# Performance work log

Measured on AMD Instinct MI355X. Metric: run time of the kernel, lower is better.

Reference implementation:

```python
import jax, jax.numpy as jnp
import numpy as np
from jax import lax

N_QUBITS = 8
DIM = 256  # 2**8 amplitudes
NUM_BLOCKS = 16
DEPTH = 1
ALPHA = 0.5
BATCH = 512

# Z-sign tables: qubit 0 is the most-significant bit of the flattened state index
_bits = (np.arange(DIM)[:, None] >> (N_QUBITS - 1 - np.arange(N_QUBITS))) & 1  # (256, 8)
_SIGNS = jnp.asarray(1.0 - 2.0 * _bits, dtype=jnp.float32)  # (256, 8)
_pairs = [(i, j) for i in range(N_QUBITS) for j in range(i + 1, N_QUBITS)]
_PAIR_SIGNS = jnp.stack([_SIGNS[:, i] * _SIGNS[:, j] for (i, j) in _pairs], axis=1)  # (256, 28)


def _apply_ry(state, c, s, q):
    # state: (N, 256) real (RY and CNOT keep the state real); gate on qubit q
    dl, dr = 2 ** q, 2 ** (N_QUBITS - 1 - q)
    st = state.reshape(-1, dl, 2, dr)
    s0, s1 = st[:, :, 0, :], st[:, :, 1, :]
    c_, s_ = c[:, None, None], s[:, None, None]
    n0 = c_ * s0 - s_ * s1
    n1 = s_ * s0 + c_ * s1
    return jnp.stack([n0, n1], axis=2).reshape(-1, DIM)


def _apply_cnot_chain(state, i):
    # CNOT control=i, target=i+1 (adjacent qubits)
    dl, dr = 2 ** i, 2 ** (N_QUBITS - 2 - i)
    st = state.reshape(-1, dl, 2, 2, dr)
    c0 = st[:, :, 0]                  # control=0: unchanged
    c1 = st[:, :, 1][:, :, ::-1]      # control=1: flip target bit
    return jnp.stack([c0, c1], axis=2).reshape(-1, DIM)


def _quantum_map(theta):
    # theta: (N, 8) -> (N, 36) [Z_i expectations (8) then Z_i Z_j for i<j (28)]
    half = 0.5 * theta
    c, s = jnp.cos(half), jnp.sin(half)
    state = jnp.zeros((theta.shape[0], DIM), dtype=theta.dtype).at[:, 0].set(1.0)
    for q in range(N_QUBITS):
        state = _apply_ry(state, c[:, q], s[:, q], q)
    for _ in range(DEPTH):
        for i in range(N_QUBITS - 1):
            state = _apply_cnot_chain(state, i)
    p = state * state  # probabilities (state is real)
    single = p @ _SIGNS          # (N, 8)
    two_body = p @ _PAIR_SIGNS   # (N, 28)
    return jnp.concatenate([single, two_body], axis=1)


def _bn(x, g, b, m, v):
    # inference-mode BatchNorm2d, eps=1e-5
    inv = g / jnp.sqrt(v + 1e-5)
    return x * inv[None, :, None, None] + (b - m * inv)[None, :, None, None]


def _conv(x, w, b):
    y = lax.conv_general_dilated(x, w, (1, 1), 'SAME',
                                 dimension_numbers=('NCHW', 'OIHW', 'NCHW'))
    return y + b[None, :, None, None]


def _maxpool2(x):
    return lax.reduce_window(x, -jnp.inf, lax.max, (1, 1, 2, 2), (1, 1, 2, 2), 'VALID')


def setup_inputs() -> dict:
    key = jax.random.key(0)
    ks = jax.random.split(key, 8)
    f32 = jnp.float32
    return {
        'x': jax.random.normal(ks[0], (BATCH, 3, 64, 64), dtype=f32),
        'conv1_w': jax.random.normal(ks[1], (16, 3, 3, 3), dtype=f32) * 0.1,
        'conv1_b': jnp.zeros((16,), f32),
        'bn1_g': jnp.ones((16,), f32), 'bn1_b': jnp.zeros((16,), f32),
        'bn1_m': jnp.zeros((16,), f32), 'bn1_v': jnp.ones((16,), f32),
        'conv2_w': jax.random.normal(ks[2], (32, 16, 3, 3), dtype=f32) * 0.08,
        'conv2_b': jnp.zeros((32,), f32),
        'bn2_g': jnp.ones((32,), f32), 'bn2_b': jnp.zeros((32,), f32),
        'bn2_m': jnp.zeros((32,), f32), 'bn2_v': jnp.ones((32,), f32),
        'conv3_w': jax.random.normal(ks[3], (64, 32, 3, 3), dtype=f32) * 0.06,
        'conv3_b': jnp.zeros((64,), f32),
        'bn3_g': jnp.ones((64,), f32), 'bn3_b': jnp.zeros((64,), f32),
        'bn3_m': jnp.zeros((64,), f32), 'bn3_v': jnp.ones((64,), f32),
        'proj_w': jax.random.normal(ks[4], (NUM_BLOCKS, 256, N_QUBITS), dtype=f32) * 0.06,
        'proj_b': jnp.zeros((NUM_BLOCKS, N_QUBITS), f32),
        'cls_w': jax.random.normal(ks[5], (10, NUM_BLOCKS * 36), dtype=f32) * 0.04,
        'cls_b': jnp.zeros((10,), f32),
    }


def reference(x, conv1_w, conv1_b, bn1_g, bn1_b, bn1_m, bn1_v,
              conv2_w, conv2_b, bn2_g, bn2_b, bn2_m, bn2_v,
              conv3_w, conv3_b, bn3_g, bn3_b, bn3_m, bn3_v,
              proj_w, proj_b, cls_w, cls_b):
    h = _maxpool2(jax.nn.relu(_bn(_conv(x, conv1_w, conv1_b), bn1_g, bn1_b, bn1_m, bn1_v)))
    h = _maxpool2(jax.nn.relu(_bn(_conv(h, conv2_w, conv2_b), bn2_g, bn2_b, bn2_m, bn2_v)))
    h = _maxpool2(jax.nn.relu(_bn(_conv(h, conv3_w, conv3_b), bn3_g, bn3_b, bn3_m, bn3_v)))
    B = h.shape[0]
    feats = h.reshape(B, NUM_BLOCKS, 256)  # 16 chunks of 256
    z = jnp.einsum('bkc,kcd->bkd', feats, proj_w) + proj_b[None]  # (B, 16, 8)
    theta = ALPHA * jnp.tanh(z)
    q_out = _quantum_map(theta.reshape(B * NUM_BLOCKS, N_QUBITS))  # (B*16, 36)
    combined = q_out.reshape(B, NUM_BLOCKS * 36)
    return combined @ cls_w.T + cls_b
```

## Files before the change

### kernel.cpp

```cpp
#include <hip/hip_runtime.h>
#include <hip/hip_bf16.h>
#include <math.h>

typedef __attribute__((ext_vector_type(8))) short short8;
typedef __attribute__((ext_vector_type(4))) float f32x4;

__device__ __forceinline__ unsigned short f2bf(float f) {
    union { float f; unsigned u; } x; x.f = f;
    unsigned r = x.u + 0x7FFF + ((x.u >> 16) & 1);
    return (unsigned short)(r >> 16);
}

__device__ __forceinline__ short8 mk8(uint2 a, uint2 b) {
    union { uint2 u[2]; short8 s; } x;
    x.u[0] = a; x.u[1] = b;
    return x.s;
}

__global__ void k_prep(const float* __restrict__ w2, const float* __restrict__ w3,
    const float* g2, const float* be2, const float* m2, const float* v2, const float* cb2,
    const float* g3, const float* be3, const float* m3, const float* v3, const float* cb3,
    const float* __restrict__ w1,
    const float* g1, const float* be1, const float* m1, const float* v1, const float* cb1,
    const float* __restrict__ pjw,
    unsigned short* __restrict__ wp2, unsigned short* __restrict__ wp3,
    unsigned short* __restrict__ wp1,
    float* __restrict__ cst2, float* __restrict__ cst3, float* __restrict__ cst1,
    float* __restrict__ pjwt)
{
    int tid = blockIdx.x * 256 + threadIdx.x;
    if (tid < 5120) {
        int j = tid & 7, lane = (tid >> 3) & 63, o = (tid >> 9) & 1, s = tid >> 10;
        int kl = ((lane >> 4) << 3) + j;
        int tp = s * 2 + (kl >> 4);
        int ic = kl & 15;
        int oc = o * 16 + (lane & 15);
        float val = (tp < 9) ? w2[(oc * 16 + ic) * 9 + tp] : 0.f;
        wp2[tid] = f2bf(val);
    } else if (tid < 23552) {
        int idx = tid - 5120;
        int j = idx & 7, lane = (idx >> 3) & 63, o = (idx >> 9) & 3, tap = idx >> 11;
        int ic = ((lane >> 4) << 3) + j;
        int oc = o * 16 + (lane & 15);
        wp3[idx] = f2bf(w3[(oc * 32 + ic) * 9 + tap]);
    } else if (tid < 23648) {
        int c = tid - 23552;
        if (c < 32) {
            float inv = g2[c] * rsqrtf(v2[c] + 1e-5f);
            cst2[c] = inv;
            cst2[32 + c] = (cb2[c] - m2[c]) * inv + be2[c];
        } else {
            int c3 = c - 32;
            float inv = g3[c3] * rsqrtf(v3[c3] + 1e-5f);
            cst3[c3] = inv;
            cst3[64 + c3] = (cb3[c3] - m3[c3]) * inv + be3[c3];
        }
    } else if (tid < 24672) {
        int idx = tid - 23648;
        int j = idx & 7, lane = (idx >> 3) & 63, s = (idx >> 9) & 1;
        int k = ((lane >> 4) << 3) + j;
        int oc = lane & 15;
        float val = 0.f;
        if (s == 0) {
            int tap = k >> 2, ic = k & 3;
            if (ic < 3) val = w1[(oc * 3 + ic) * 9 + tap];
        } else {
            if (k < 3) val = w1[(oc * 3 + k) * 9 + 8];
        }
        wp1[idx] = f2bf(val);
    } else if (tid < 24688) {
        int c = tid - 24672;
        float inv = g1[c] * rsqrtf(v1[c] + 1e-5f);
        cst1[c] = inv;
        cst1[16 + c] = (cb1[c] - m1[c]) * inv + be1[c];
    } else if (tid < 57456) {
        int idx = tid - 24688;
        int k = idx >> 11, d = (idx >> 8) & 7, c = idx & 255;
        pjwt[idx] = pjw[k * 2048 + c * 8 + d];
    }
}

__global__ __launch_bounds__(512, 4) void k_fused(
    const float* __restrict__ x,
    const unsigned short* __restrict__ wp1, const float* __restrict__ cst1,
    const unsigned short* __restrict__ wp2, const float* __restrict__ cst2,
    const unsigned short* __restrict__ wp3, const float* __restrict__ cst3,
    const float* __restrict__ pjwt, const float* __restrict__ pjb,
    const float* __restrict__ cw, const float* __restrict__ cbias,
    float* __restrict__ out)
{
    __shared__ __align__(16) unsigned char smem[57728];
    unsigned short* xs   = (unsigned short*)smem;
    unsigned short* h2tA = (unsigned short*)smem;
    unsigned short* h2tB = (unsigned short*)(smem + 10368);
    unsigned short* h1A  = (unsigned short*)(smem + 20736);
    unsigned short* h1B  = (unsigned short*)(smem + 39232);
    float* feats = (float*)(smem + 20736);
    float* czs   = (float*)(smem + 20736 + 17408);
    float* partl = czs + 128;

    int b = blockIdx.x, t = threadIdx.x;
    int lane = t & 63, w = t >> 6, q = lane >> 4, xl = lane & 15;
    const float* img = x + (size_t)b * 12288;

    if (t < 264) {
        int arr = t & 1, idx = t >> 1;
        int y, xx;
        if (idx < 34)       { y = 0;        xx = idx; }
        else if (idx < 68)  { y = 33;       xx = idx - 34; }
        else if (idx < 100) { y = idx - 67; xx = 0; }
        else                { y = idx - 99; xx = 33; }
        uint4 z = {0u, 0u, 0u, 0u};
        *(uint4*)((arr ? h1B : h1A) + (y * 34 + xx) * 8) = z;
    }

    short8 A10 = *(const short8*)(wp1 + (lane << 3));
    short8 A11 = *(const short8*)(wp1 + ((64 + lane) << 3));
    int t0 = 2 * q, t1 = 2 * q + 1;
    int dy0 = t0 / 3 - 1, dx0 = t0 % 3 - 1;
    int dy1 = t1 / 3 - 1, dx1 = t1 % 3 - 1;
    float inv1[4], bs1[4];
    #pragma unroll
    for (int reg = 0; reg < 4; ++reg) {
        inv1[reg] = cst1[q * 4 + reg];
        bs1[reg]  = cst1[16 + q * 4 + reg];
    }
    unsigned* h1w = (unsigned*)(q < 2 ? h1A : h1B);
    #pragma unroll 1
    for (int h = 0; h < 2; ++h) {
        if (h) __syncthreads();
        int y0 = h * 32 - 1;
        #pragma unroll 1
        for (int i = 0; i < 5; ++i) {
            int idx = t + i * 512;
            if (idx < 2244) {
                int y = idx / 66, xx = idx - y * 66;
                int gy = y0 + y, gx = xx - 1;
                float v0 = 0.f, v1 = 0.f, v2 = 0.f;
                if ((unsigned)gy < 64u && (unsigned)gx < 64u) {
                    const float* pb = img + gy * 64 + gx;
                    v0 = pb[0]; v1 = pb[4096]; v2 = pb[8192];
                }
                uint2 pk;
                pk.x = (unsigned)f2bf(v0) | ((unsigned)f2bf(v1) << 16);
                pk.y = (unsigned)f2bf(v2);
                ((uint2*)xs)[idx] = pk;
            }
        }
        __syncthreads();
        #pragma unroll 1
        for (int xT = 0; xT < 4; ++xT) {
            int xb = xT * 16 + xl + 1;
            float pv[4], vo[4];
            #pragma unroll
            for (int r = 0; r < 4; ++r) {
                int ly = w * 4 + r + 1;
                const uint2* base = (const uint2*)xs;
                uint2 ua = base[(ly + dy0) * 66 + xb + dx0];
                uint2 ub = base[(ly + dy1) * 66 + xb + dx1];
                uint2 uc = base[(ly + 1) * 66 + xb + 1];
                f32x4 acc = (f32x4){0.f, 0.f, 0.f, 0.f};
                acc = __builtin_amdgcn_mfma_f32_16x16x32_bf16(A10, mk8(ua, ub), acc, 0, 0, 0);
                acc = __builtin_amdgcn_mfma_f32_16x16x32_bf16(A11, mk8(uc, uc), acc, 0, 0, 0);
                #pragma unroll
                for (int reg = 0; reg < 4; ++reg) {
                    float val = fmaxf(acc[reg] * inv1[reg] + bs1[reg], 0.f);
                    if (r & 1) {
                        float vm = fmaxf(val, pv[reg]);
                        vo[reg] = fmaxf(vm, __shfl_xor(vm, 1, 64));
                    } else {
                        pv[reg] = val;
                    }
                }
                if ((r & 1) && !(lane & 1)) {
                    int py = h * 16 + w * 2 + (r >> 1);
                    int px = xT * 8 + (xl >> 1);
                    int pos = (py + 1) * 34 + (px + 1);
                    unsigned u0 = (unsigned)f2bf(vo[0]) | ((unsigned)f2bf(vo[1]) << 16);
                    unsigned u1 = (unsigned)f2bf(vo[2]) | ((unsigned)f2bf(vo[3]) << 16);
                    unsigned* hp = h1w + pos * 4 + (q & 1) * 2;
                    hp[0] = u0; hp[1] = u1;
                }
            }
        }
    }
    __syncthreads();

    if (t < 264) {
        int idx = t >> 1, half = t & 1;
        int y, xx;
        if (idx < 18)      { y = 0;        xx = idx; }
        else if (idx < 36) { y = 17;       xx = idx - 18; }
        else if (idx < 52) { y = idx - 35; xx = 0; }
        else if (idx < 68) { y = idx - 51; xx = 17; }
        else { y = -1; xx = 0; }
        if (y >= 0) {
            uint4 z = {0u, 0u, 0u, 0u};
            int pos = y * 18 + xx;
            *(uint4*)((half ? h2tB : h2tA) + pos * 16) = z;
            *(uint4*)((half ? h2tB : h2tA) + pos * 16 + 8) = z;
        }
    }
    short8 A2[5][2];
    #pragma unroll
    for (int s = 0; s < 5; ++s)
        #pragma unroll
        for (int o = 0; o < 2; ++o)
            A2[s][o] = *(const short8*)(wp2 + (((s * 2 + o) * 64 + lane) << 3));
    int dyA[5], dxA[5];
    #pragma unroll
    for (int s = 0; s < 5; ++s) {
        int tp = s * 2 + (q >> 1); if (tp > 8) tp = 8;
        int d3 = tp / 3;
        dyA[s] = d3 - 1; dxA[s] = tp - d3 * 3 - 1;
    }
    {
        const unsigned short* h1r = (q & 1) ? h1B : h1A;
        f32x4 acc[4][2][2];
        #pragma unroll
        for (int r = 0; r < 4; ++r)
            #pragma unroll
            for (int xT = 0; xT < 2; ++xT)
                #pragma unroll
                for (int o = 0; o < 2; ++o)
                    acc[r][xT][o] = (f32x4){0.f, 0.f, 0.f, 0.f};
        #pragma unroll
        for (int r = 0; r < 4; ++r) {
            int ry = w * 4 + r;
            #pragma unroll
            for (int xT = 0; xT < 2; ++xT) {
                int gxb = xT * 16 + xl;
                #pragma unroll
                for (int s = 0; s < 5; ++s) {
                    int pos = (ry + dyA[s] + 1) * 34 + (gxb + dxA[s] + 1);
                    short8 B = *(const short8*)(h1r + pos * 8);
                    acc[r][xT][0] = __builtin_amdgcn_mfma_f32_16x16x32_bf16(A2[s][0], B, acc[r][xT][0], 0, 0, 0);
                    acc[r][xT][1] = __builtin_amdgcn_mfma_f32_16x16x32_bf16(A2[s][1], B, acc[r][xT][1], 0, 0, 0);
                }
            }
        }
        #pragma unroll
        for (int oT = 0; oT < 2; ++oT)
            #pragma unroll
            for (int rp = 0; rp < 2; ++rp)
                #pragma unroll
                for (int xT = 0; xT < 2; ++xT) {
                    float vo[4];
                    #pragma unroll
                    for (int reg = 0; reg < 4; ++reg) {
                        int oc = oT * 16 + q * 4 + reg;
                        float inv = cst2[oc], bs = cst2[32 + oc];
                        float v0 = fmaxf(acc[rp * 2][xT][oT][reg] * inv + bs, 0.f);
                        float v1 = fmaxf(acc[rp * 2 + 1][xT][oT][reg] * inv + bs, 0.f);
                        float vm = fmaxf(v0, v1);
                        vo[reg] = fmaxf(vm, __shfl_xor(vm, 1, 64));
                    }
                    if (!(lane & 1)) {
                        int py = w * 2 + rp;
                        int px = xT * 8 + (xl >> 1);
                        int pos = (py + 1) * 18 + (px + 1);
                        unsigned u0 = (unsigned)f2bf(vo[0]) | ((unsigned)f2bf(vo[1]) << 16);
                        unsigned u1 = (unsigned)f2bf(vo[2]) | ((unsigned)f2bf(vo[3]) << 16);
                        unsigned* hp = (unsigned*)(oT ? h2tB : h2tA) + pos * 8 + q * 2;
                        hp[0] = u0; hp[1] = u1;
                    }
                }
    }
    __syncthreads();

    {
        int op = w & 1, rg = w >> 1;
        const unsigned short* h2r = (q < 2) ? h2tA : h2tB;
        short8 A3[9][2];
        #pragma unroll
        for (int tap = 0; tap < 9; ++tap)
            #pragma unroll
            for (int tt = 0; tt < 2; ++tt)
                A3[tap][tt] = *(const short8*)(wp3 + (((tap * 4 + op * 2 + tt) * 64 + lane) << 3));
        f32x4 acc[4][2];
        #pragma unroll
        for (int r = 0; r < 4; ++r) {
            acc[r][0] = (f32x4){0.f, 0.f, 0.f, 0.f};
            acc[r][1] = (f32x4){0.f, 0.f, 0.f, 0.f};
        }
        #pragma unroll
        for (int r = 0; r < 4; ++r) {
            int ry = rg * 4 + r + 1;
            #pragma unroll
            for (int tap = 0; tap < 9; ++tap) {
                int pos = (ry + tap / 3 - 1) * 18 + xl + (tap % 3);
                short8 B = *(const short8*)(h2r + pos * 16 + (q & 1) * 8);
                acc[r][0] = __builtin_amdgcn_mfma_f32_16x16x32_bf16(A3[tap][0], B, acc[r][0], 0, 0, 0);
                acc[r][1] = __builtin_amdgcn_mfma_f32_16x16x32_bf16(A3[tap][1], B, acc[r][1], 0, 0, 0);
            }
        }
        #pragma unroll
        for (int tt = 0; tt < 2; ++tt)
            #pragma unroll
            for (int reg = 0; reg < 4; ++reg) {
                int oc = (op * 2 + tt) * 16 + q * 4 + reg;
                float inv = cst3[oc], bs = cst3[64 + oc];
                #pragma unroll
                for (int rp = 0; rp < 2; ++rp) {
                    float v0 = fmaxf(acc[rp * 2][tt][reg] * inv + bs, 0.f);
                    float v1 = fmaxf(acc[rp * 2 + 1][tt][reg] * inv + bs, 0.f);
                    float vm = fmaxf(v0, v1);
                    float vv = fmaxf(vm, __shfl_xor(vm, 1, 64));
                    if (!(lane & 1))
                        feats[oc * 68 + (rg * 2 + rp) * 8 + (xl >> 1)] = vv;
                }
            }
    }
    __syncthreads();

    if (t < 128) {
        int k = t >> 3, d = t & 7;
        const float4* wrow = (const float4*)(pjwt + (k * 8 + d) * 256);
        float zacc = 0.f;
        #pragma unroll 4
        for (int i = 0; i < 64; ++i) {
            int c4 = (i + k) & 63;
            float4 wv = wrow[c4];
            const float* fp = &feats[(k * 4 + (c4 >> 4)) * 68 + 4 * (c4 & 15)];
            float4 fv = *(const float4*)fp;
            zacc = fmaf(wv.x, fv.x, zacc);
            zacc = fmaf(wv.y, fv.y, zacc);
            zacc = fmaf(wv.z, fv.z, zacc);
            zacc = fmaf(wv.w, fv.w, zacc);
        }
        float z = zacc + pjb[k * 8 + d];
        czs[k * 8 + d] = cosf(0.5f * tanhf(z));
    }
    __syncthreads();
    if (t < 160) {
        int k = t / 10, c = t - (t / 10) * 10;
        float cz[8];
        #pragma unroll
        for (int i = 0; i < 8; ++i) cz[i] = czs[k * 8 + i];
        const float* cwp = cw + c * 576 + k * 36;
        float s = 0.f;
        float pp = 1.f;
        #pragma unroll
        for (int i = 0; i < 8; ++i) { pp *= cz[i]; s = fmaf(pp, cwp[i], s); }
        int cnt = 8;
        #pragma unroll
        for (int i = 0; i < 8; ++i) {
            float p2 = 1.f;
            #pragma unroll
            for (int j = i + 1; j < 8; ++j) { p2 *= cz[j]; s = fmaf(p2, cwp[cnt++], s); }
        }
        partl[k * 10 + c] = s;
    }
    __syncthreads();
    if (t < 10) {
        float s = cbias[t];
        #pragma unroll
        for (int k = 0; k < 16; ++k) s += partl[k * 10 + t];
        out[b * 10 + t] = s;
    }
}

extern "C" void kernel_launch(void* const* d_in, const int* in_sizes, int n_in,
                              void* d_out, int out_size, void* d_ws, size_t ws_size,
                              hipStream_t stream) {
    const float* x     = (const float*)d_in[0];
    const float* c1w   = (const float*)d_in[1];
    const float* c1b   = (const float*)d_in[2];
    const float* b1g   = (const float*)d_in[3];
    const float* b1b   = (const float*)d_in[4];
    const float* b1m   = (const float*)d_in[5];
    const float* b1v   = (const float*)d_in[6];
    const float* c2w   = (const float*)d_in[7];
    const float* c2b   = (const float*)d_in[8];
    const float* b2g   = (const float*)d_in[9];
    const float* b2b   = (const float*)d_in[10];
    const float* b2m   = (const float*)d_in[11];
    const float* b2v   = (const float*)d_in[12];
    const float* c3w   = (const float*)d_in[13];
    const float* c3b   = (const float*)d_in[14];
    const float* b3g   = (const float*)d_in[15];
    const float* b3b   = (const float*)d_in[16];
    const float* b3m   = (const float*)d_in[17];
    const float* b3v   = (const float*)d_in[18];
    const float* pjw   = (const float*)d_in[19];
    const float* pjb   = (const float*)d_in[20];
    const float* cw    = (const float*)d_in[21];
    const float* cbias = (const float*)d_in[22];
    float* outp = (float*)d_out;

    unsigned char* prep = (unsigned char*)d_ws;
    unsigned short* wp2 = (unsigned short*)prep;
    unsigned short* wp3 = (unsigned short*)(prep + 16384);
    unsigned short* wp1 = (unsigned short*)(prep + 16384 + 36864);
    float* cst2 = (float*)(prep + 16384 + 36864 + 2048);
    float* cst3 = cst2 + 64;
    float* cst1 = cst3 + 128;
    float* pjwt = (float*)(prep + 16384 + 36864 + 2048 + 1024);

    k_prep<<<225, 256, 0, stream>>>(c2w, c3w, b2g, b2b, b2m, b2v, c2b,
                                    b3g, b3b, b3m, b3v, c3b,
                                    c1w, b1g, b1b, b1m, b1v, c1b, pjw,
                                    wp2, wp3, wp1, cst2, cst3, cst1, pjwt);
    k_fused<<<512, 512, 0, stream>>>(x, wp1, cst1, wp2, cst2, wp3, cst3,
                                     pjwt, pjb, cw, cbias, outp);
}
```

Before: 138.8 us.

## Switch conv2/conv3 to 32x32x16 MFMA with channel-split layouts and transposed feats

Rewrites the conv2 and conv3 stages to use 32x32x16 bf16 MFMA tiles instead of 16x16x32. The intermediate h2 is now stored as four 8-channel planes, feats is transposed to position-major, and the projection weights are permuted to match. Weights are loaded from global per tap rather than held in registers, and the conv1 loop is unrolled by two. The aim is fewer MFMA issues and less padding waste (conv2 no longer pads 9 taps to 10), in exchange for more global weight loads and different LDS access patterns.

```diff
diff --git a/kernel.cpp b/kernel.cpp
--- a/kernel.cpp
+++ b/kernel.cpp
@@ -4,6 +4,7 @@
 
 typedef __attribute__((ext_vector_type(8))) short short8;
 typedef __attribute__((ext_vector_type(4))) float f32x4;
+typedef __attribute__((ext_vector_type(16))) float f32x16;
 
 __device__ __forceinline__ unsigned short f2bf(float f) {
     union { float f; unsigned u; } x; x.f = f;
@@ -29,22 +30,20 @@
     float* __restrict__ pjwt)
 {
     int tid = blockIdx.x * 256 + threadIdx.x;
-    if (tid < 5120) {
-        int j = tid & 7, lane = (tid >> 3) & 63, o = (tid >> 9) & 1, s = tid >> 10;
-        int kl = ((lane >> 4) << 3) + j;
-        int tp = s * 2 + (kl >> 4);
-        int ic = kl & 15;
-        int oc = o * 16 + (lane & 15);
-        float val = (tp < 9) ? w2[(oc * 16 + ic) * 9 + tp] : 0.f;
-        wp2[tid] = f2bf(val);
-    } else if (tid < 23552) {
-        int idx = tid - 5120;
-        int j = idx & 7, lane = (idx >> 3) & 63, o = (idx >> 9) & 3, tap = idx >> 11;
-        int ic = ((lane >> 4) << 3) + j;
-        int oc = o * 16 + (lane & 15);
+    if (tid < 4608) {
+        int j = tid & 7, lane = (tid >> 3) & 63, tap = tid >> 9;
+        int oc = lane & 31;
+        int ic = ((lane >> 5) << 3) + j;
+        wp2[tid] = f2bf(w2[(oc * 16 + ic) * 9 + tap]);
+    } else if (tid < 23040) {
+        int idx = tid - 4608;
+        int j = idx & 7, lane = (idx >> 3) & 63;
+        int ot = (idx >> 9) & 1, h = (idx >> 10) & 1, tap = idx >> 11;
+        int oc = ot * 32 + (lane & 31);
+        int ic = h * 16 + ((lane >> 5) << 3) + j;
         wp3[idx] = f2bf(w3[(oc * 32 + ic) * 9 + tap]);
-    } else if (tid < 23648) {
-        int c = tid - 23552;
+    } else if (tid < 23136) {
+        int c = tid - 23040;
         if (c < 32) {
             float inv = g2[c] * rsqrtf(v2[c] + 1e-5f);
             cst2[c] = inv;
@@ -55,8 +54,8 @@
             cst3[c3] = inv;
             cst3[64 + c3] = (cb3[c3] - m3[c3]) * inv + be3[c3];
         }
-    } else if (tid < 24672) {
-        int idx = tid - 23648;
+    } else if (tid < 24160) {
+        int idx = tid - 23136;
         int j = idx & 7, lane = (idx >> 3) & 63, s = (idx >> 9) & 1;
         int k = ((lane >> 4) << 3) + j;
         int oc = lane & 15;
@@ -68,15 +67,15 @@
             if (k < 3) val = w1[(oc * 3 + k) * 9 + 8];
         }
         wp1[idx] = f2bf(val);
-    } else if (tid < 24688) {
-        int c = tid - 24672;
+    } else if (tid < 24176) {
+        int c = tid - 24160;
         float inv = g1[c] * rsqrtf(v1[c] + 1e-5f);
         cst1[c] = inv;
         cst1[16 + c] = (cb1[c] - m1[c]) * inv + be1[c];
-    } else if (tid < 57456) {
-        int idx = tid - 24688;
-        int k = idx >> 11, d = (idx >> 8) & 7, c = idx & 255;
-        pjwt[idx] = pjw[k * 2048 + c * 8 + d];
+    } else if (tid < 56944) {
+        int idx = tid - 24176;
+        int o = idx & 3, pos = (idx >> 2) & 63, d = (idx >> 8) & 7, k = idx >> 11;
+        pjwt[idx] = pjw[k * 2048 + (o * 64 + pos) * 8 + d];
     }
 }
 
@@ -89,15 +88,14 @@
     const float* __restrict__ cw, const float* __restrict__ cbias,
     float* __restrict__ out)
 {
-    __shared__ __align__(16) unsigned char smem[57728];
-    unsigned short* xs   = (unsigned short*)smem;
-    unsigned short* h2tA = (unsigned short*)smem;
-    unsigned short* h2tB = (unsigned short*)(smem + 10368);
-    unsigned short* h1A  = (unsigned short*)(smem + 20736);
-    unsigned short* h1B  = (unsigned short*)(smem + 39232);
-    float* feats = (float*)(smem + 20736);
-    float* czs   = (float*)(smem + 20736 + 17408);
+    __shared__ __align__(16) unsigned char smem[58880];
+    unsigned short* xs  = (unsigned short*)smem;
+    unsigned short* h2t = (unsigned short*)smem;
+    float* czs   = (float*)(smem + 20736);
     float* partl = czs + 128;
+    unsigned short* h1A = (unsigned short*)(smem + 21888);
+    unsigned short* h1B = (unsigned short*)(smem + 40384);
+    float* feats = (float*)(smem + 21888);
 
     int b = blockIdx.x, t = threadIdx.x;
     int lane = t & 63, w = t >> 6, q = lane >> 4, xl = lane & 15;
@@ -148,7 +146,7 @@
             }
         }
         __syncthreads();
-        #pragma unroll 1
+        #pragma unroll 2
         for (int xT = 0; xT < 4; ++xT) {
             int xb = xT * 16 + xl + 1;
             float pv[4], vo[4];
@@ -186,128 +184,103 @@
     }
     __syncthreads();
 
-    if (t < 264) {
-        int idx = t >> 1, half = t & 1;
+    if (t < 272) {
+        int arr = t & 3, idx = t >> 2;
         int y, xx;
         if (idx < 18)      { y = 0;        xx = idx; }
         else if (idx < 36) { y = 17;       xx = idx - 18; }
         else if (idx < 52) { y = idx - 35; xx = 0; }
-        else if (idx < 68) { y = idx - 51; xx = 17; }
-        else { y = -1; xx = 0; }
-        if (y >= 0) {
-            uint4 z = {0u, 0u, 0u, 0u};
-            int pos = y * 18 + xx;
-            *(uint4*)((half ? h2tB : h2tA) + pos * 16) = z;
-            *(uint4*)((half ? h2tB : h2tA) + pos * 16 + 8) = z;
-        }
-    }
-    short8 A2[5][2];
-    #pragma unroll
-    for (int s = 0; s < 5; ++s)
-        #pragma unroll
-        for (int o = 0; o < 2; ++o)
-            A2[s][o] = *(const short8*)(wp2 + (((s * 2 + o) * 64 + lane) << 3));
-    int dyA[5], dxA[5];
-    #pragma unroll
-    for (int s = 0; s < 5; ++s) {
-        int tp = s * 2 + (q >> 1); if (tp > 8) tp = 8;
-        int d3 = tp / 3;
-        dyA[s] = d3 - 1; dxA[s] = tp - d3 * 3 - 1;
-    }
+        else               { y = idx - 51; xx = 17; }
+        uint4 z = {0u, 0u, 0u, 0u};
+        *(uint4*)(h2t + arr * 2592 + (y * 18 + xx) * 8) = z;
+    }
+
     {
-        const unsigned short* h1r = (q & 1) ? h1B : h1A;
-        f32x4 acc[4][2][2];
-        #pragma unroll
-        for (int r = 0; r < 4; ++r)
-            #pragma unroll
-            for (int xT = 0; xT < 2; ++xT)
+        int n = lane & 31, kh = lane >> 5;
+        const unsigned short* h1r = kh ? h1B : h1A;
+        f32x16 acc2[4];
+        #pragma unroll
+        for (int r = 0; r < 4; ++r) acc2[r] = (f32x16)(0.f);
+        #pragma unroll
+        for (int tap = 0; tap < 9; ++tap) {
+            short8 A = *(const short8*)(wp2 + ((tap * 64 + lane) << 3));
+            int dy = tap / 3 - 1, dx = tap % 3 - 1;
+            int pbase = (w * 4 + dy + 1) * 34 + (n + dx + 1);
+            #pragma unroll
+            for (int r = 0; r < 4; ++r) {
+                short8 B = *(const short8*)(h1r + (pbase + r * 34) * 8);
+                acc2[r] = __builtin_amdgcn_mfma_f32_32x32x16_bf16(A, B, acc2[r], 0, 0, 0);
+            }
+        }
+        #pragma unroll
+        for (int g = 0; g < 4; ++g) {
+            int oc0 = g * 8 + kh * 4;
+            float4 inv = *(const float4*)&cst2[oc0];
+            float4 bsv = *(const float4*)&cst2[32 + oc0];
+            #pragma unroll
+            for (int rg = 0; rg < 2; ++rg) {
+                float vo[4];
                 #pragma unroll
-                for (int o = 0; o < 2; ++o)
-                    acc[r][xT][o] = (f32x4){0.f, 0.f, 0.f, 0.f};
-        #pragma unroll
-        for (int r = 0; r < 4; ++r) {
-            int ry = w * 4 + r;
-            #pragma unroll
-            for (int xT = 0; xT < 2; ++xT) {
-                int gxb = xT * 16 + xl;
+                for (int j = 0; j < 4; ++j) {
+                    int reg = g * 4 + j;
+                    float iv = ((const float*)&inv)[j], bv = ((const float*)&bsv)[j];
+                    float v0 = fmaxf(acc2[rg * 2][reg] * iv + bv, 0.f);
+                    float v1 = fmaxf(acc2[rg * 2 + 1][reg] * iv + bv, 0.f);
+                    float vm = fmaxf(v0, v1);
+                    vo[j] = fmaxf(vm, __shfl_xor(vm, 1, 64));
+                }
+                if (!(n & 1)) {
+                    int py = w * 2 + rg, px = n >> 1;
+                    int pos = (py + 1) * 18 + (px + 1);
+                    unsigned u0 = (unsigned)f2bf(vo[0]) | ((unsigned)f2bf(vo[1]) << 16);
+                    unsigned u1 = (unsigned)f2bf(vo[2]) | ((unsigned)f2bf(vo[3]) << 16);
+                    unsigned* hp = (unsigned*)(h2t + g * 2592 + pos * 8 + kh * 4);
+                    hp[0] = u0; hp[1] = u1;
+                }
+            }
+        }
+    }
+    __syncthreads();
+
+    {
+        int n = lane & 31, kh = lane >> 5;
+        int yr = n >> 4, px_ = n & 15;
+        f32x16 acc3[2];
+        acc3[0] = (f32x16)(0.f);
+        acc3[1] = (f32x16)(0.f);
+        #pragma unroll
+        for (int tap = 0; tap < 9; ++tap) {
+            int dy = tap / 3 - 1, dx = tap % 3 - 1;
+            int pos = (2 * w + yr + dy + 1) * 18 + (px_ + dx + 1);
+            #pragma unroll
+            for (int h = 0; h < 2; ++h) {
+                short8 B = *(const short8*)(h2t + (h * 2 + kh) * 2592 + pos * 8);
+                short8 A0 = *(const short8*)(wp3 + ((((tap * 2 + h) * 2 + 0) * 64 + lane) << 3));
+                short8 A1 = *(const short8*)(wp3 + ((((tap * 2 + h) * 2 + 1) * 64 + lane) << 3));
+                acc3[0] = __builtin_amdgcn_mfma_f32_32x32x16_bf16(A0, B, acc3[0], 0, 0, 0);
+                acc3[1] = __builtin_amdgcn_mfma_f32_32x32x16_bf16(A1, B, acc3[1], 0, 0, 0);
+            }
+        }
+        #pragma unroll
+        for (int ot = 0; ot < 2; ++ot)
+            #pragma unroll
+            for (int g = 0; g < 4; ++g) {
+                int oc0 = ot * 32 + g * 8 + kh * 4;
+                float4 inv = *(const float4*)&cst3[oc0];
+                float4 bsv = *(const float4*)&cst3[64 + oc0];
+                float vo[4];
                 #pragma unroll
-                for (int s = 0; s < 5; ++s) {
-                    int pos = (ry + dyA[s] + 1) * 34 + (gxb + dxA[s] + 1);
-                    short8 B = *(const short8*)(h1r + pos * 8);
-                    acc[r][xT][0] = __builtin_amdgcn_mfma_f32_16x16x32_bf16(A2[s][0], B, acc[r][xT][0], 0, 0, 0);
-                    acc[r][xT][1] = __builtin_amdgcn_mfma_f32_16x16x32_bf16(A2[s][1], B, acc[r][xT][1], 0, 0, 0);
-                }
-            }
-        }
-        #pragma unroll
-        for (int oT = 0; oT < 2; ++oT)
-            #pragma unroll
-            for (int rp = 0; rp < 2; ++rp)
-                #pragma unroll
-                for (int xT = 0; xT < 2; ++xT) {
-                    float vo[4];
-                    #pragma unroll
-                    for (int reg = 0; reg < 4; ++reg) {
-                        int oc = oT * 16 + q * 4 + reg;
-                        float inv = cst2[oc], bs = cst2[32 + oc];
-                        float v0 = fmaxf(acc[rp * 2][xT][oT][reg] * inv + bs, 0.f);
-                        float v1 = fmaxf(acc[rp * 2 + 1][xT][oT][reg] * inv + bs, 0.f);
-                        float vm = fmaxf(v0, v1);
-                        vo[reg] = fmaxf(vm, __shfl_xor(vm, 1, 64));
-                    }
-                    if (!(lane & 1)) {
-                        int py = w * 2 + rp;
-                        int px = xT * 8 + (xl >> 1);
-                        int pos = (py + 1) * 18 + (px + 1);
-                        unsigned u0 = (unsigned)f2bf(vo[0]) | ((unsigned)f2bf(vo[1]) << 16);
-                        unsigned u1 = (unsigned)f2bf(vo[2]) | ((unsigned)f2bf(vo[3]) << 16);
-                        unsigned* hp = (unsigned*)(oT ? h2tB : h2tA) + pos * 8 + q * 2;
-                        hp[0] = u0; hp[1] = u1;
-                    }
-                }
-    }
-    __syncthreads();
-
-    {
-        int op = w & 1, rg = w >> 1;
-        const unsigned short* h2r = (q < 2) ? h2tA : h2tB;
-        short8 A3[9][2];
-        #pragma unroll
-        for (int tap = 0; tap < 9; ++tap)
-            #pragma unroll
-            for (int tt = 0; tt < 2; ++tt)
-                A3[tap][tt] = *(const short8*)(wp3 + (((tap * 4 + op * 2 + tt) * 64 + lane) << 3));
-        f32x4 acc[4][2];
-        #pragma unroll
-        for (int r = 0; r < 4; ++r) {
-            acc[r][0] = (f32x4){0.f, 0.f, 0.f, 0.f};
-            acc[r][1] = (f32x4){0.f, 0.f, 0.f, 0.f};
-        }
-        #pragma unroll
-        for (int r = 0; r < 4; ++r) {
-            int ry = rg * 4 + r + 1;
-            #pragma unroll
-            for (int tap = 0; tap < 9; ++tap) {
-                int pos = (ry + tap / 3 - 1) * 18 + xl + (tap % 3);
-                short8 B = *(const short8*)(h2r + pos * 16 + (q & 1) * 8);
-                acc[r][0] = __builtin_amdgcn_mfma_f32_16x16x32_bf16(A3[tap][0], B, acc[r][0], 0, 0, 0);
-                acc[r][1] = __builtin_amdgcn_mfma_f32_16x16x32_bf16(A3[tap][1], B, acc[r][1], 0, 0, 0);
-            }
-        }
-        #pragma unroll
-        for (int tt = 0; tt < 2; ++tt)
-            #pragma unroll
-            for (int reg = 0; reg < 4; ++reg) {
-                int oc = (op * 2 + tt) * 16 + q * 4 + reg;
-                float inv = cst3[oc], bs = cst3[64 + oc];
-                #pragma unroll
-                for (int rp = 0; rp < 2; ++rp) {
-                    float v0 = fmaxf(acc[rp * 2][tt][reg] * inv + bs, 0.f);
-                    float v1 = fmaxf(acc[rp * 2 + 1][tt][reg] * inv + bs, 0.f);
-                    float vm = fmaxf(v0, v1);
-                    float vv = fmaxf(vm, __shfl_xor(vm, 1, 64));
-                    if (!(lane & 1))
-                        feats[oc * 68 + (rg * 2 + rp) * 8 + (xl >> 1)] = vv;
+                for (int j = 0; j < 4; ++j) {
+                    int reg = g * 4 + j;
+                    float iv = ((const float*)&inv)[j], bv = ((const float*)&bsv)[j];
+                    float v = fmaxf(acc3[ot][reg] * iv + bv, 0.f);
+                    float vy = fmaxf(v, __shfl_xor(v, 16, 64));
+                    vo[j] = fmaxf(vy, __shfl_xor(vy, 1, 64));
+                }
+                if (!(n & 17)) {
+                    int pos = w * 8 + (px_ >> 1);
+                    float4 pk = {vo[0], vo[1], vo[2], vo[3]};
+                    *(float4*)&feats[pos * 68 + oc0] = pk;
                 }
             }
     }
@@ -315,14 +288,12 @@
 
     if (t < 128) {
         int k = t >> 3, d = t & 7;
-        const float4* wrow = (const float4*)(pjwt + (k * 8 + d) * 256);
+        const float4* wrow = (const float4*)(pjwt + ((k * 8 + d) << 8));
         float zacc = 0.f;
         #pragma unroll 4
-        for (int i = 0; i < 64; ++i) {
-            int c4 = (i + k) & 63;
-            float4 wv = wrow[c4];
-            const float* fp = &feats[(k * 4 + (c4 >> 4)) * 68 + 4 * (c4 & 15)];
-            float4 fv = *(const float4*)fp;
+        for (int pos = 0; pos < 64; ++pos) {
+            float4 wv = wrow[pos];
+            float4 fv = *(const float4*)&feats[pos * 68 + k * 4];
             zacc = fmaf(wv.x, fv.x, zacc);
             zacc = fmaf(wv.y, fv.y, zacc);
             zacc = fmaf(wv.z, fv.z, zacc);
@@ -397,7 +368,7 @@
     float* cst1 = cst3 + 128;
     float* pjwt = (float*)(prep + 16384 + 36864 + 2048 + 1024);
 
-    k_prep<<<225, 256, 0, stream>>>(c2w, c3w, b2g, b2b, b2m, b2v, c2b,
+    k_prep<<<223, 256, 0, stream>>>(c2w, c3w, b2g, b2b, b2m, b2v, c2b,
                                     b3g, b3b, b3m, b3v, c3b,
                                     c1w, b1g, b1b, b1m, b1v, c1b, pjw,
                                     wp2, wp3, wp1, cst2, cst3, cst1, pjwt);
```

Result: slower. 142.9 us (+3.0%).

## Shrink padded LDS tiles and cut register pressure to raise occupancy

Applied to the files above, without the earlier changes.

Drops the right and bottom padding rows and columns from the conv1 and conv2 output tiles (34→33, 18→17 strides). Reads that fall out of range are redirected to a shared zero row or column, so the LDS footprint shrinks. The conv2 and conv3 weight fragments are now loaded per tap inside the loop instead of being held in registers, and conv2 accumulators are split per x-tile. Launch bounds go from 4 to 6 waves-per-SIMD hint so more blocks can be resident. The trade is more global/L2 weight loads and extra index selects per MFMA in exchange for fewer VGPRs and less LDS.

```diff
diff --git a/kernel.cpp b/kernel.cpp
--- a/kernel.cpp
+++ b/kernel.cpp
@@ -80,7 +80,7 @@
     }
 }
 
-__global__ __launch_bounds__(512, 4) void k_fused(
+__global__ __launch_bounds__(512, 6) void k_fused(
     const float* __restrict__ x,
     const unsigned short* __restrict__ wp1, const float* __restrict__ cst1,
     const unsigned short* __restrict__ wp2, const float* __restrict__ cst2,
@@ -89,29 +89,26 @@
     const float* __restrict__ cw, const float* __restrict__ cbias,
     float* __restrict__ out)
 {
-    __shared__ __align__(16) unsigned char smem[57728];
+    __shared__ __align__(16) unsigned char smem[53344];
     unsigned short* xs   = (unsigned short*)smem;
     unsigned short* h2tA = (unsigned short*)smem;
-    unsigned short* h2tB = (unsigned short*)(smem + 10368);
-    unsigned short* h1A  = (unsigned short*)(smem + 20736);
-    unsigned short* h1B  = (unsigned short*)(smem + 39232);
-    float* feats = (float*)(smem + 20736);
-    float* czs   = (float*)(smem + 20736 + 17408);
-    float* partl = czs + 128;
+    unsigned short* h2tB = (unsigned short*)(smem + 9248);
+    float* czs   = (float*)smem;
+    float* partl = (float*)(smem + 512);
+    unsigned short* h1A = (unsigned short*)(smem + 18496);
+    unsigned short* h1B = (unsigned short*)(smem + 35920);
+    float* feats = (float*)(smem + 18496);
 
     int b = blockIdx.x, t = threadIdx.x;
     int lane = t & 63, w = t >> 6, q = lane >> 4, xl = lane & 15;
     const float* img = x + (size_t)b * 12288;
 
-    if (t < 264) {
-        int arr = t & 1, idx = t >> 1;
+    if (t < 130) {
+        int arr = t & 1, p = t >> 1;
         int y, xx;
-        if (idx < 34)       { y = 0;        xx = idx; }
-        else if (idx < 68)  { y = 33;       xx = idx - 34; }
-        else if (idx < 100) { y = idx - 67; xx = 0; }
-        else                { y = idx - 99; xx = 33; }
+        if (p < 33) { y = 0; xx = p; } else { y = p - 32; xx = 0; }
         uint4 z = {0u, 0u, 0u, 0u};
-        *(uint4*)((arr ? h1B : h1A) + (y * 34 + xx) * 8) = z;
+        *(uint4*)((arr ? h1B : h1A) + (y * 33 + xx) * 8) = z;
     }
 
     short8 A10 = *(const short8*)(wp1 + (lane << 3));
@@ -148,7 +145,7 @@
             }
         }
         __syncthreads();
-        #pragma unroll 1
+        #pragma unroll 2
         for (int xT = 0; xT < 4; ++xT) {
             int xb = xT * 16 + xl + 1;
             float pv[4], vo[4];
@@ -175,7 +172,7 @@
                 if ((r & 1) && !(lane & 1)) {
                     int py = h * 16 + w * 2 + (r >> 1);
                     int px = xT * 8 + (xl >> 1);
-                    int pos = (py + 1) * 34 + (px + 1);
+                    int pos = (py + 1) * 33 + (px + 1);
                     unsigned u0 = (unsigned)f2bf(vo[0]) | ((unsigned)f2bf(vo[1]) << 16);
                     unsigned u1 = (unsigned)f2bf(vo[2]) | ((unsigned)f2bf(vo[3]) << 16);
                     unsigned* hp = h1w + pos * 4 + (q & 1) * 2;
@@ -186,97 +183,78 @@
     }
     __syncthreads();
 
-    if (t < 264) {
-        int idx = t >> 1, half = t & 1;
+    if (t < 66) {
+        int arr = t & 1, p = t >> 1;
         int y, xx;
-        if (idx < 18)      { y = 0;        xx = idx; }
-        else if (idx < 36) { y = 17;       xx = idx - 18; }
-        else if (idx < 52) { y = idx - 35; xx = 0; }
-        else if (idx < 68) { y = idx - 51; xx = 17; }
-        else { y = -1; xx = 0; }
-        if (y >= 0) {
-            uint4 z = {0u, 0u, 0u, 0u};
-            int pos = y * 18 + xx;
-            *(uint4*)((half ? h2tB : h2tA) + pos * 16) = z;
-            *(uint4*)((half ? h2tB : h2tA) + pos * 16 + 8) = z;
-        }
-    }
-    short8 A2[5][2];
-    #pragma unroll
-    for (int s = 0; s < 5; ++s)
-        #pragma unroll
-        for (int o = 0; o < 2; ++o)
-            A2[s][o] = *(const short8*)(wp2 + (((s * 2 + o) * 64 + lane) << 3));
-    int dyA[5], dxA[5];
-    #pragma unroll
-    for (int s = 0; s < 5; ++s) {
-        int tp = s * 2 + (q >> 1); if (tp > 8) tp = 8;
-        int d3 = tp / 3;
-        dyA[s] = d3 - 1; dxA[s] = tp - d3 * 3 - 1;
-    }
+        if (p < 17) { y = 0; xx = p; } else { y = p - 16; xx = 0; }
+        uint4 z = {0u, 0u, 0u, 0u};
+        uint4* bp = (uint4*)((arr ? h2tB : h2tA) + (y * 17 + xx) * 16);
+        bp[0] = z; bp[1] = z;
+    }
+
     {
         const unsigned short* h1r = (q & 1) ? h1B : h1A;
-        f32x4 acc[4][2][2];
-        #pragma unroll
-        for (int r = 0; r < 4; ++r)
-            #pragma unroll
-            for (int xT = 0; xT < 2; ++xT)
+        int dyA[5], dxA[5];
+        #pragma unroll
+        for (int s = 0; s < 5; ++s) {
+            int tp = s * 2 + (q >> 1); if (tp > 8) tp = 8;
+            int d3 = tp / 3;
+            dyA[s] = d3 - 1; dxA[s] = tp - d3 * 3 - 1;
+        }
+        #pragma unroll 1
+        for (int xT = 0; xT < 2; ++xT) {
+            f32x4 acc[4][2];
+            #pragma unroll
+            for (int r = 0; r < 4; ++r) {
+                acc[r][0] = (f32x4){0.f, 0.f, 0.f, 0.f};
+                acc[r][1] = (f32x4){0.f, 0.f, 0.f, 0.f};
+            }
+            #pragma unroll
+            for (int s = 0; s < 5; ++s) {
+                short8 A0 = *(const short8*)(wp2 + (((s * 2 + 0) * 64 + lane) << 3));
+                short8 A1 = *(const short8*)(wp2 + (((s * 2 + 1) * 64 + lane) << 3));
                 #pragma unroll
-                for (int o = 0; o < 2; ++o)
-                    acc[r][xT][o] = (f32x4){0.f, 0.f, 0.f, 0.f};
-        #pragma unroll
-        for (int r = 0; r < 4; ++r) {
-            int ry = w * 4 + r;
-            #pragma unroll
-            for (int xT = 0; xT < 2; ++xT) {
-                int gxb = xT * 16 + xl;
+                for (int r = 0; r < 4; ++r) {
+                    int gy = w * 4 + r + dyA[s];
+                    int gx = xT * 16 + xl + dxA[s];
+                    int rowI = ((unsigned)gy < 32u) ? gy + 1 : 0;
+                    int colI = ((unsigned)gx < 32u) ? gx + 1 : 0;
+                    short8 B = *(const short8*)(h1r + (rowI * 33 + colI) * 8);
+                    acc[r][0] = __builtin_amdgcn_mfma_f32_16x16x32_bf16(A0, B, acc[r][0], 0, 0, 0);
+                    acc[r][1] = __builtin_amdgcn_mfma_f32_16x16x32_bf16(A1, B, acc[r][1], 0, 0, 0);
+                }
+            }
+            #pragma unroll
+            for (int oT = 0; oT < 2; ++oT)
                 #pragma unroll
-                for (int s = 0; s < 5; ++s) {
-                    int pos = (ry + dyA[s] + 1) * 34 + (gxb + dxA[s] + 1);
-                    short8 B = *(const short8*)(h1r + pos * 8);
-                    acc[r][xT][0] = __builtin_amdgcn_mfma_f32_16x16x32_bf16(A2[s][0], B, acc[r][xT][0], 0, 0, 0);
-                    acc[r][xT][1] = __builtin_amdgcn_mfma_f32_16x16x32_bf16(A2[s][1], B, acc[r][xT][1], 0, 0, 0);
-                }
-            }
-        }
-        #pragma unroll
-        for (int oT = 0; oT < 2; ++oT)
-            #pragma unroll
-            for (int rp = 0; rp < 2; ++rp)
-                #pragma unroll
-                for (int xT = 0; xT < 2; ++xT) {
+                for (int rp = 0; rp < 2; ++rp) {
                     float vo[4];
                     #pragma unroll
                     for (int reg = 0; reg < 4; ++reg) {
                         int oc = oT * 16 + q * 4 + reg;
-                        float inv = cst2[oc], bs = cst2[32 + oc];
-                        float v0 = fmaxf(acc[rp * 2][xT][oT][reg] * inv + bs, 0.f);
-                        float v1 = fmaxf(acc[rp * 2 + 1][xT][oT][reg] * inv + bs, 0.f);
+                        float iv = cst2[oc], bv = cst2[32 + oc];
+                        float v0 = fmaxf(acc[rp * 2][oT][reg] * iv + bv, 0.f);
+                        float v1 = fmaxf(acc[rp * 2 + 1][oT][reg] * iv + bv, 0.f);
                         float vm = fmaxf(v0, v1);
                         vo[reg] = fmaxf(vm, __shfl_xor(vm, 1, 64));
                     }
                     if (!(lane & 1)) {
-                        int py = w * 2 + rp;
-                        int px = xT * 8 + (xl >> 1);
-                        int pos = (py + 1) * 18 + (px + 1);
+                        int py = w * 2 + rp, px = xT * 8 + (xl >> 1);
+                        int pos = (py + 1) * 17 + (px + 1);
                         unsigned u0 = (unsigned)f2bf(vo[0]) | ((unsigned)f2bf(vo[1]) << 16);
                         unsigned u1 = (unsigned)f2bf(vo[2]) | ((unsigned)f2bf(vo[3]) << 16);
                         unsigned* hp = (unsigned*)(oT ? h2tB : h2tA) + pos * 8 + q * 2;
                         hp[0] = u0; hp[1] = u1;
                     }
                 }
+        }
     }
     __syncthreads();
 
     {
         int op = w & 1, rg = w >> 1;
         const unsigned short* h2r = (q < 2) ? h2tA : h2tB;
-        short8 A3[9][2];
-        #pragma unroll
-        for (int tap = 0; tap < 9; ++tap)
-            #pragma unroll
-            for (int tt = 0; tt < 2; ++tt)
-                A3[tap][tt] = *(const short8*)(wp3 + (((tap * 4 + op * 2 + tt) * 64 + lane) << 3));
+        int icoff = (q & 1) * 8;
         f32x4 acc[4][2];
         #pragma unroll
         for (int r = 0; r < 4; ++r) {
@@ -284,14 +262,19 @@
             acc[r][1] = (f32x4){0.f, 0.f, 0.f, 0.f};
         }
         #pragma unroll
-        for (int r = 0; r < 4; ++r) {
-            int ry = rg * 4 + r + 1;
-            #pragma unroll
-            for (int tap = 0; tap < 9; ++tap) {
-                int pos = (ry + tap / 3 - 1) * 18 + xl + (tap % 3);
-                short8 B = *(const short8*)(h2r + pos * 16 + (q & 1) * 8);
-                acc[r][0] = __builtin_amdgcn_mfma_f32_16x16x32_bf16(A3[tap][0], B, acc[r][0], 0, 0, 0);
-                acc[r][1] = __builtin_amdgcn_mfma_f32_16x16x32_bf16(A3[tap][1], B, acc[r][1], 0, 0, 0);
+        for (int tap = 0; tap < 9; ++tap) {
+            short8 A0 = *(const short8*)(wp3 + (((tap * 4 + op * 2 + 0) * 64 + lane) << 3));
+            short8 A1 = *(const short8*)(wp3 + (((tap * 4 + op * 2 + 1) * 64 + lane) << 3));
+            int dy = tap / 3 - 1, dx = tap % 3 - 1;
+            int cx = xl + dx;
+            int colI = ((unsigned)cx < 16u) ? cx + 1 : 0;
+            #pragma unroll
+            for (int r = 0; r < 4; ++r) {
+                int cy = rg * 4 + r + dy;
+                int rowI = ((unsigned)cy < 16u) ? cy + 1 : 0;
+                short8 B = *(const short8*)(h2r + (rowI * 17 + colI) * 16 + icoff);
+                acc[r][0] = __builtin_amdgcn_mfma_f32_16x16x32_bf16(A0, B, acc[r][0], 0, 0, 0);
+                acc[r][1] = __builtin_amdgcn_mfma_f32_16x16x32_bf16(A1, B, acc[r][1], 0, 0, 0);
             }
         }
         #pragma unroll
@@ -299,11 +282,11 @@
             #pragma unroll
             for (int reg = 0; reg < 4; ++reg) {
                 int oc = (op * 2 + tt) * 16 + q * 4 + reg;
-                float inv = cst3[oc], bs = cst3[64 + oc];
+                float iv = cst3[oc], bv = cst3[64 + oc];
                 #pragma unroll
                 for (int rp = 0; rp < 2; ++rp) {
-                    float v0 = fmaxf(acc[rp * 2][tt][reg] * inv + bs, 0.f);
-                    float v1 = fmaxf(acc[rp * 2 + 1][tt][reg] * inv + bs, 0.f);
+                    float v0 = fmaxf(acc[rp * 2][tt][reg] * iv + bv, 0.f);
+                    float v1 = fmaxf(acc[rp * 2 + 1][tt][reg] * iv + bv, 0.f);
                     float vm = fmaxf(v0, v1);
                     float vv = fmaxf(vm, __shfl_xor(vm, 1, 64));
                     if (!(lane & 1))
@@ -315,7 +298,7 @@
 
     if (t < 128) {
         int k = t >> 3, d = t & 7;
-        const float4* wrow = (const float4*)(pjwt + (k * 8 + d) * 256);
+        const float4* wrow = (const float4*)(pjwt + ((k * 8 + d) << 8));
         float zacc = 0.f;
         #pragma unroll 4
         for (int i = 0; i < 64; ++i) {
```

Result: slower. 170.3 us (+22.7%).

## Prefetch conv1 image halves into registers and overlap with MFMA compute

Applied to the files above, without the earlier changes.

The second half of the input image is now loaded into registers while the first half's conv1 MFMA work runs, so the global loads are no longer serialized behind a barrier. The change also switches bf16 packing to the paired hardware conversion intrinsic, unrolls the conv1 x-tile loop by two, and splits the projection dot product into four independent accumulators to shorten the dependency chain. The cost is higher register pressure from holding 15 prefetched floats per thread, which may reduce occupancy. Summation order in the projection changes slightly.

```diff
diff --git a/kernel.cpp b/kernel.cpp
--- a/kernel.cpp
+++ b/kernel.cpp
@@ -9,6 +9,12 @@
     union { float f; unsigned u; } x; x.f = f;
     unsigned r = x.u + 0x7FFF + ((x.u >> 16) & 1);
     return (unsigned short)(r >> 16);
+}
+
+__device__ __forceinline__ unsigned pk2bf(float a, float b) {
+    union { __hip_bfloat162 h; unsigned u; } x;
+    x.h = __float22bfloat162_rn(make_float2(a, b));
+    return x.u;
 }
 
 __device__ __forceinline__ short8 mk8(uint2 a, uint2 b) {
@@ -126,29 +132,53 @@
         bs1[reg]  = cst1[16 + q * 4 + reg];
     }
     unsigned* h1w = (unsigned*)(q < 2 ? h1A : h1B);
+
+    float sv0[5], sv1[5], sv2[5];
+    #pragma unroll
+    for (int i = 0; i < 5; ++i) {
+        int idx = t + i * 512;
+        float v0 = 0.f, v1 = 0.f, v2 = 0.f;
+        if (idx < 2244) {
+            int y = idx / 66, xx = idx - y * 66;
+            int gy = y - 1, gx = xx - 1;
+            if ((unsigned)gy < 64u && (unsigned)gx < 64u) {
+                const float* pb = img + gy * 64 + gx;
+                v0 = pb[0]; v1 = pb[4096]; v2 = pb[8192];
+            }
+        }
+        sv0[i] = v0; sv1[i] = v1; sv2[i] = v2;
+    }
+
     #pragma unroll 1
     for (int h = 0; h < 2; ++h) {
-        if (h) __syncthreads();
-        int y0 = h * 32 - 1;
-        #pragma unroll 1
+        #pragma unroll
         for (int i = 0; i < 5; ++i) {
             int idx = t + i * 512;
             if (idx < 2244) {
-                int y = idx / 66, xx = idx - y * 66;
-                int gy = y0 + y, gx = xx - 1;
+                uint2 pk;
+                pk.x = pk2bf(sv0[i], sv1[i]);
+                pk.y = pk2bf(sv2[i], 0.f);
+                ((uint2*)xs)[idx] = pk;
+            }
+        }
+        __syncthreads();
+        if (h == 0) {
+            #pragma unroll
+            for (int i = 0; i < 5; ++i) {
+                int idx = t + i * 512;
                 float v0 = 0.f, v1 = 0.f, v2 = 0.f;
-                if ((unsigned)gy < 64u && (unsigned)gx < 64u) {
-                    const float* pb = img + gy * 64 + gx;
-                    v0 = pb[0]; v1 = pb[4096]; v2 = pb[8192];
-                }
-                uint2 pk;
-                pk.x = (unsigned)f2bf(v0) | ((unsigned)f2bf(v1) << 16);
-                pk.y = (unsigned)f2bf(v2);
-                ((uint2*)xs)[idx] = pk;
-            }
-        }
-        __syncthreads();
-        #pragma unroll 1
+                if (idx < 2244) {
+                    int y = idx / 66, xx = idx - y * 66;
+                    int gy = 31 + y, gx = xx - 1;
+                    if ((unsigned)gy < 64u && (unsigned)gx < 64u) {
+                        const float* pb = img + gy * 64 + gx;
+                        v0 = pb[0]; v1 = pb[4096]; v2 = pb[8192];
+                    }
+                }
+                sv0[i] = v0; sv1[i] = v1; sv2[i] = v2;
+            }
+        }
+        #pragma unroll 2
         for (int xT = 0; xT < 4; ++xT) {
             int xb = xT * 16 + xl + 1;
             float pv[4], vo[4];
@@ -176,15 +206,14 @@
                     int py = h * 16 + w * 2 + (r >> 1);
                     int px = xT * 8 + (xl >> 1);
                     int pos = (py + 1) * 34 + (px + 1);
-                    unsigned u0 = (unsigned)f2bf(vo[0]) | ((unsigned)f2bf(vo[1]) << 16);
-                    unsigned u1 = (unsigned)f2bf(vo[2]) | ((unsigned)f2bf(vo[3]) << 16);
                     unsigned* hp = h1w + pos * 4 + (q & 1) * 2;
-                    hp[0] = u0; hp[1] = u1;
-                }
-            }
-        }
-    }
-    __syncthreads();
+                    hp[0] = pk2bf(vo[0], vo[1]);
+                    hp[1] = pk2bf(vo[2], vo[3]);
+                }
+            }
+        }
+        __syncthreads();
+    }
 
     if (t < 264) {
         int idx = t >> 1, half = t & 1;
@@ -259,10 +288,9 @@
                         int py = w * 2 + rp;
                         int px = xT * 8 + (xl >> 1);
                         int pos = (py + 1) * 18 + (px + 1);
-                        unsigned u0 = (unsigned)f2bf(vo[0]) | ((unsigned)f2bf(vo[1]) << 16);
-                        unsigned u1 = (unsigned)f2bf(vo[2]) | ((unsigned)f2bf(vo[3]) << 16);
                         unsigned* hp = (unsigned*)(oT ? h2tB : h2tA) + pos * 8 + q * 2;
-                        hp[0] = u0; hp[1] = u1;
+                        hp[0] = pk2bf(vo[0], vo[1]);
+                        hp[1] = pk2bf(vo[2], vo[3]);
                     }
                 }
     }
@@ -315,20 +343,23 @@
 
     if (t < 128) {
         int k = t >> 3, d = t & 7;
-        const float4* wrow = (const float4*)(pjwt + (k * 8 + d) * 256);
-        float zacc = 0.f;
+        const float4* wrow = (const float4*)(pjwt + ((k * 8 + d) << 8));
+        float za[4] = {0.f, 0.f, 0.f, 0.f};
         #pragma unroll 4
-        for (int i = 0; i < 64; ++i) {
-            int c4 = (i + k) & 63;
-            float4 wv = wrow[c4];
-            const float* fp = &feats[(k * 4 + (c4 >> 4)) * 68 + 4 * (c4 & 15)];
-            float4 fv = *(const float4*)fp;
-            zacc = fmaf(wv.x, fv.x, zacc);
-            zacc = fmaf(wv.y, fv.y, zacc);
-            zacc = fmaf(wv.z, fv.z, zacc);
-            zacc = fmaf(wv.w, fv.w, zacc);
-        }
-        float z = zacc + pjb[k * 8 + d];
+        for (int i = 0; i < 16; ++i) {
+            #pragma unroll
+            for (int j = 0; j < 4; ++j) {
+                int c4 = (i + j * 16 + k) & 63;
+                float4 wv = wrow[c4];
+                const float* fp = &feats[(k * 4 + (c4 >> 4)) * 68 + 4 * (c4 & 15)];
+                float4 fv = *(const float4*)fp;
+                za[j] = fmaf(wv.x, fv.x, za[j]);
+                za[j] = fmaf(wv.y, fv.y, za[j]);
+                za[j] = fmaf(wv.z, fv.z, za[j]);
+                za[j] = fmaf(wv.w, fv.w, za[j]);
+            }
+        }
+        float z = (za[0] + za[1]) + (za[2] + za[3]) + pjb[k * 8 + d];
         czs[k * 8 + d] = cosf(0.5f * tanhf(z));
     }
     __syncthreads();
```

After: 141.2 us. About the same (+1.7%).
